# Optimization experiments

Hardware: AMD Instinct MI355X
Metric: run time of the kernel (lower is better)

The kernel has to match this reference:

```python
import jax, jax.numpy as jnp
import numpy as np

H = 8          # n_heads
C_FACTOR = 3   # autocorrelation factor c
KS = 25        # series-decomp moving-average kernel


def series_decomp(x, ks=KS):
    # AvgPool1d(kernel=ks, stride=1, pad=ks//2), count_include_pad=True (torch default)
    p = ks // 2
    xp = jnp.pad(x, ((0, 0), (p, p), (0, 0)))            # [B, L+2p, D]
    cs = jnp.pad(jnp.cumsum(xp, axis=1), ((0, 0), (1, 0), (0, 0)))
    trend = (cs[:, ks:, :] - cs[:, :-ks, :]) / ks         # [B, L, D]
    return x - trend, trend


def auto_correlation(x, Wq, bq, Wk, bk, Wv, bv):
    B, L, D = x.shape
    d = D // H

    def proj(W, b):  # [B,L,D] -> [B,H,L,d]
        return (x @ W + b).reshape(B, L, H, d).transpose(0, 2, 1, 3)

    Q, K, V = proj(Wq, bq), proj(Wk, bk), proj(Wv, bv)
    Qf = jnp.fft.rfft(Q, axis=2)
    Kf = jnp.fft.rfft(K, axis=2)
    Corr = jnp.fft.irfft(Qf * jnp.conj(Kf), n=L, axis=2)  # [B,H,L,d]

    k = int(C_FACTOR * np.log(L))                         # topk = int(c*log(L))
    C2 = Corr.transpose(0, 1, 3, 2)                       # [B,H,d,L] - topk along lag axis per channel
    W_topk, I_topk = jax.lax.top_k(C2, k)                 # [B,H,d,k]
    W_topk = jax.nn.softmax(W_topk, axis=-1)

    # saturating shift: pos = min(delay + t, L-1)  (faithful to clamp(max=L-1))
    t = jnp.arange(L)
    pos = jnp.minimum(I_topk[..., None] + t[None, None, None, None, :], L - 1)  # [B,H,d,k,L]
    Vt = V.transpose(0, 1, 3, 2)                          # [B,H,d,L]
    gathered = jnp.take_along_axis(Vt[:, :, :, None, :], pos, axis=4)           # [B,H,d,k,L]
    R = jnp.einsum('bhdk,bhdkl->bhdl', W_topk, gathered)  # weighted aggregate over lags
    return R.transpose(0, 3, 1, 2).reshape(B, L, D)       # [B,L,D]


def setup_inputs() -> dict:
    key = jax.random.key(0)
    ks = jax.random.split(key, 11)
    B, L, D = 8, 1024, 512
    s = 0.02
    return {
        'x':  jax.random.normal(ks[0], (B, L, D), jnp.float32),
        'Wq': jax.random.normal(ks[1], (D, D), jnp.float32) * s,
        'bq': jnp.zeros((D,), jnp.float32),
        'Wk': jax.random.normal(ks[2], (D, D), jnp.float32) * s,
        'bk': jnp.zeros((D,), jnp.float32),
        'Wv': jax.random.normal(ks[3], (D, D), jnp.float32) * s,
        'bv': jnp.zeros((D,), jnp.float32),
        'W1': jax.random.normal(ks[4], (D, D), jnp.float32) * s,
        'b1': jnp.zeros((D,), jnp.float32),
        'W2': jax.random.normal(ks[5], (D, D), jnp.float32) * s,
        'b2': jnp.zeros((D,), jnp.float32),
    }


def reference(x, Wq, bq, Wk, bk, Wv, bv, W1, b1, W2, b2):
    attn = auto_correlation(x, Wq, bq, Wk, bk, Wv, bv)
    x_s, _ = series_decomp(attn + x)
    y = jax.nn.relu(x_s @ W1 + b1) @ W2 + b2              # FFN (dropout is identity in eval)
    x_s, _ = series_decomp(y + x_s)
    return x_s
```

## Files before the change

### kernel.cpp

```cpp
#include <hip/hip_runtime.h>
#include <math.h>

#define LL 1024
#define DD 512
#define NB 8
#define KTOP 20
#define SZ (8 * 512 * 1024)

typedef __attribute__((ext_vector_type(8))) short bf16x8;
typedef __attribute__((ext_vector_type(4))) float f32x4;
typedef __attribute__((ext_vector_type(4))) int i32x4;

__device__ __forceinline__ unsigned short f2bf(float f) {
  union { float f; unsigned u; } v; v.f = f;
  unsigned r = v.u + 0x7FFFu + ((v.u >> 16) & 1u);
  return (unsigned short)(r >> 16);
}
__device__ __forceinline__ float bf2f(unsigned short u) {
  union { unsigned u; float f; } v; v.u = ((unsigned)u) << 16;
  return v.f;
}

__device__ __forceinline__ void gload16(const void* g, void* l) {
  __builtin_amdgcn_global_load_lds(
      (const __attribute__((address_space(1))) unsigned int*)g,
      (__attribute__((address_space(3))) unsigned int*)l, 16, 0, 0);
}

__global__ __launch_bounds__(256) void k_prep(const float* __restrict__ x,
                                              unsigned short* __restrict__ xbT,
                                              unsigned short* __restrict__ xb,
                                              const float* __restrict__ Wq,
                                              const float* __restrict__ Wk,
                                              const float* __restrict__ Wv,
                                              const float* __restrict__ W1,
                                              const float* __restrict__ W2,
                                              const float* __restrict__ bq,
                                              const float* __restrict__ bk,
                                              const float* __restrict__ bv,
                                              unsigned short* __restrict__ WqkvT,
                                              unsigned short* __restrict__ W1T,
                                              unsigned short* __restrict__ W2T,
                                              float* __restrict__ bqkv) {
  __shared__ float T[64][65];
  int bid = blockIdx.x;
  int tid = threadIdx.x;
  int lane = tid & 63, r4 = tid >> 6;
  if (bid < 1024) {
    int b = bid >> 7, c0 = ((bid >> 4) & 7) * 64, t0 = (bid & 15) * 64;
#pragma unroll
    for (int it = 0; it < 16; ++it) {
      int tl = it * 4 + r4;
      T[lane][tl] = x[((size_t)b * LL + t0 + tl) * DD + c0 + lane];
    }
    __syncthreads();
#pragma unroll
    for (int it = 0; it < 16; ++it) {
      int cl = it * 4 + r4;
      xbT[((size_t)b * DD + c0 + cl) * LL + t0 + lane] = f2bf(T[cl][lane]);
    }
    int tl2 = tid >> 2, cq = (tid & 3) * 16;
    unsigned short* dxb = xb + ((size_t)b * LL + t0 + tl2) * DD + c0 + cq;
#pragma unroll
    for (int j = 0; j < 16; j += 4) {
      ushort4 u;
      u.x = f2bf(T[cq + j][tl2]);
      u.y = f2bf(T[cq + j + 1][tl2]);
      u.z = f2bf(T[cq + j + 2][tl2]);
      u.w = f2bf(T[cq + j + 3][tl2]);
      *(ushort4*)&dxb[j] = u;
    }
  } else {
    int pid = bid - 1024;
    int z = pid >> 6, n0 = ((pid >> 3) & 7) * 64, k0 = (pid & 7) * 64;
    const float* W = (z == 0) ? Wq : (z == 1) ? Wk : (z == 2) ? Wv : (z == 3) ? W1 : W2;
    unsigned short* dst = (z == 0) ? WqkvT
                        : (z == 1) ? (WqkvT + 512 * 512)
                        : (z == 2) ? (WqkvT + 1024 * 512)
                        : (z == 3) ? W1T : W2T;
#pragma unroll
    for (int it = 0; it < 16; ++it) {
      int kl = it * 4 + r4;
      T[lane][kl] = W[(size_t)(k0 + kl) * DD + n0 + lane];
    }
    __syncthreads();
    int n = tid >> 2, kq = (tid & 3) * 16;
    unsigned short* d = dst + (size_t)(n0 + n) * DD + k0 + kq;
#pragma unroll
    for (int j = 0; j < 16; j += 4) {
      ushort4 u;
      u.x = f2bf(T[n][kq + j]);
      u.y = f2bf(T[n][kq + j + 1]);
      u.z = f2bf(T[n][kq + j + 2]);
      u.w = f2bf(T[n][kq + j + 3]);
      *(ushort4*)&d[j] = u;
    }
    if (z == 4 && n0 == 0 && k0 == 0) {
      for (int i = tid; i < 1536; i += 256) {
        const float* s = (i < 512) ? bq : (i < 1024) ? bk : bv;
        bqkv[i] = s[i & 511];
      }
    }
  }
}

template <int MODE, int BM>
__global__ __launch_bounds__(256) void k_mfma(const unsigned short* __restrict__ Aptr,
                                              const unsigned short* __restrict__ Bt,
                                              const float* __restrict__ bias,
                                              const unsigned short* __restrict__ resbT,
                                              unsigned short* __restrict__ outU,
                                              float* __restrict__ outF, int gx) {
  constexpr int MI = BM / 32;
  __shared__ char smem[(BM + 128) * 64 * 2 + (BM == 128 ? 2048 : 0)];
  unsigned short* As = (unsigned short*)smem;
  unsigned short* Bs = (unsigned short*)(smem + BM * 128);
  float* Cs = (float*)smem;

  int tid = threadIdx.x;
  int lane = tid & 63, wid = tid >> 6;
  int wr = wid & 1, wc = wid >> 1;

  int nwg = gridDim.x;
  int wg = blockIdx.x;
  int swz = (wg & 7) * (nwg >> 3) + (wg >> 3);
  int bix = swz % gx, biy = swz / gx;
  int n0 = bix * 128, m0 = biy * BM;
  int b = m0 >> 10, t0 = m0 & (LL - 1);

  f32x4 acc[MI][4];
#pragma unroll
  for (int i = 0; i < MI; ++i)
#pragma unroll
    for (int j = 0; j < 4; ++j) acc[i][j] = (f32x4){0.f, 0.f, 0.f, 0.f};

  int srow = tid >> 3, sq = tid & 7;

  for (int k0 = 0; k0 < 512; k0 += 64) {
#pragma unroll
    for (int p = 0; p < MI; ++p) {
      int r = srow + p * 32;
      int dq = sq ^ (r & 7);
      gload16(Aptr + (size_t)(m0 + r) * 512 + k0 + dq * 8, &As[r * 64 + sq * 8]);
    }
#pragma unroll
    for (int p = 0; p < 4; ++p) {
      int r = srow + p * 32;
      int dq = sq ^ (r & 7);
      gload16(Bt + (size_t)(n0 + r) * 512 + k0 + dq * 8, &Bs[r * 64 + sq * 8]);
    }
    __syncthreads();
#pragma unroll
    for (int ks = 0; ks < 2; ++ks) {
      bf16x8 af[MI], bf[4];
      int fr = lane & 15, kq = lane >> 4;
#pragma unroll
      for (int mi = 0; mi < MI; ++mi) {
        int r = wr * (BM / 2) + mi * 16 + fr;
        af[mi] = *(bf16x8*)&As[r * 64 + ((ks * 4 + kq) ^ (r & 7)) * 8];
      }
#pragma unroll
      for (int ni = 0; ni < 4; ++ni) {
        int r = wc * 64 + ni * 16 + fr;
        bf[ni] = *(bf16x8*)&Bs[r * 64 + ((ks * 4 + kq) ^ (r & 7)) * 8];
      }
#pragma unroll
      for (int mi = 0; mi < MI; ++mi)
#pragma unroll
        for (int ni = 0; ni < 4; ++ni)
          acc[mi][ni] = __builtin_amdgcn_mfma_f32_16x16x32_bf16(af[mi], bf[ni], acc[mi][ni], 0, 0, 0);
    }
    __syncthreads();
  }

  if (MODE == 0) {
    const int LDc = 132;
    for (int p = 0; p < 2; ++p) {
      __syncthreads();
      if (wc == p) {
#pragma unroll
        for (int mi = 0; mi < MI; ++mi)
#pragma unroll
          for (int ni = 0; ni < 4; ++ni) {
            int nl = ni * 16 + (lane & 15);
            int ml = wr * (BM / 2) + mi * 16 + (lane >> 4) * 4;
            *(f32x4*)&Cs[nl * LDc + ml] = acc[mi][ni];
          }
      }
      __syncthreads();
      {
        int n = tid >> 2, mq = tid & 3;
        int ng = n0 + p * 64 + n;
        float bv = bias[ng];
        int sel = ng >> 9;
        unsigned short* drow =
            outU + ((size_t)sel * NB * 512 + b * 512 + (ng & 511)) * LL + t0;
#pragma unroll
        for (int i = 0; i < 8; ++i) {
          int m = mq * 4 + i * 16;
          float4 v = *(float4*)&Cs[n * LDc + m];
          ushort4 u;
          u.x = f2bf(v.x + bv); u.y = f2bf(v.y + bv);
          u.z = f2bf(v.z + bv); u.w = f2bf(v.w + bv);
          *(ushort4*)&drow[m] = u;
        }
      }
    }
  } else if (MODE == 2) {
    const int LDc = 68;
    for (int p = 0; p < 2; ++p) {
      __syncthreads();
      {
        int n = tid >> 2, mq = tid & 3;
        const unsigned short* rrow =
            resbT + ((size_t)(b * 512) + n0 + p * 64 + n) * LL + t0;
#pragma unroll
        for (int i = 0; i < 4; ++i) {
          int m = mq * 16 + i * 4;
          ushort4 u = *(const ushort4*)&rrow[m];
          float4 v;
          v.x = bf2f(u.x); v.y = bf2f(u.y); v.z = bf2f(u.z); v.w = bf2f(u.w);
          *(float4*)&Cs[n * LDc + m] = v;
        }
      }
      __syncthreads();
      if (wc == p) {
#pragma unroll
        for (int mi = 0; mi < MI; ++mi)
#pragma unroll
          for (int ni = 0; ni < 4; ++ni) {
            int nl = ni * 16 + (lane & 15);
            int ml = wr * (BM / 2) + mi * 16 + (lane >> 4) * 4;
            f32x4 cur = *(f32x4*)&Cs[nl * LDc + ml];
            cur += acc[mi][ni];
            *(f32x4*)&Cs[nl * LDc + ml] = cur;
          }
      }
      __syncthreads();
      {
        int n = tid >> 2, mq = tid & 3;
        int ng = n0 + p * 64 + n;
        float bv = bias[ng];
        float* drow = outF + ((size_t)b * 512 + ng) * LL + t0;
#pragma unroll
        for (int i = 0; i < 4; ++i) {
          int m = mq * 16 + i * 4;
          float4 v = *(float4*)&Cs[n * LDc + m];
          v.x += bv; v.y += bv; v.z += bv; v.w += bv;
          *(float4*)&drow[m] = v;
        }
      }
    }
  } else {
    const int LDh = 68;
    for (int p = 0; p < 2; ++p) {
      __syncthreads();
      if (wc == p) {
#pragma unroll
        for (int mi = 0; mi < MI; ++mi)
#pragma unroll
          for (int ni = 0; ni < 4; ++ni) {
            int nl = ni * 16 + (lane & 15);
            int ml = wr * (BM / 2) + mi * 16 + (lane >> 4) * 4;
#pragma unroll
            for (int r = 0; r < 4; ++r) Cs[(ml + r) * LDh + nl] = acc[mi][ni][r];
          }
      }
      __syncthreads();
      {
        int m = tid >> 2, nh = tid & 3;
        unsigned short* drow =
            outU + (size_t)(m0 + m) * 512 + n0 + p * 64 + nh * 16;
#pragma unroll
        for (int c = 0; c < 4; ++c) {
          float4 v = *(float4*)&Cs[m * LDh + nh * 16 + c * 4];
          float4 bb = *(const float4*)&bias[n0 + p * 64 + nh * 16 + c * 4];
          v.x = fmaxf(v.x + bb.x, 0.f);
          v.y = fmaxf(v.y + bb.y, 0.f);
          v.z = fmaxf(v.z + bb.z, 0.f);
          v.w = fmaxf(v.w + bb.w, 0.f);
          ushort4 u;
          u.x = f2bf(v.x); u.y = f2bf(v.y); u.z = f2bf(v.z); u.w = f2bf(v.w);
          *(ushort4*)&drow[c * 4] = u;
        }
      }
    }
  }
}

__global__ __launch_bounds__(256, 8) void k_autocorr(const unsigned short* __restrict__ Qbf,
                                                     const unsigned short* __restrict__ Kbf,
                                                     const unsigned short* __restrict__ Vbf,
                                                     const unsigned short* __restrict__ xbT,
                                                     unsigned short* __restrict__ xsbT) {
  __shared__ char sm[16672];
  unsigned* KshW = (unsigned*)sm;
  float* Vs2 = (float*)(sm + 8320);
  float* wvs = (float*)(sm + 16512);
  int*   wis = (int*)(sm + 16592);
  float* Csp = (float*)sm;
  float* Cp  = (float*)(sm + 4224);

  int tid = threadIdx.x;
  int lane = tid & 63, wave = tid >> 6;
  size_t base = (size_t)blockIdx.x * LL;

  {
    ushort4 vv = *(const ushort4*)(Vbf + base + tid * 4);
    float4 vf;
    vf.x = bf2f(vv.x); vf.y = bf2f(vv.y); vf.z = bf2f(vv.z); vf.w = bf2f(vv.w);
    *(float4*)&Vs2[tid * 4] = vf;
    float vlast = bf2f(Vbf[base + 1023]);
    *(float4*)&Vs2[1024 + tid * 4] = make_float4(vlast, vlast, vlast, vlast);

    ushort4 kv = *(const ushort4*)(Kbf + base + tid * 4);
    unsigned w0 = (unsigned)kv.x | ((unsigned)kv.y << 16);
    unsigned w1 = (unsigned)kv.z | ((unsigned)kv.w << 16);
    unsigned wq = __shfl_up(w0, 1);
    unsigned wp = __shfl_up(w1, 1);
    if (lane == 0) {
      wq = *(const unsigned*)(Kbf + base + ((tid * 4 - 4) & (LL - 1)));
      wp = *(const unsigned*)(Kbf + base + ((tid * 4 - 2) & (LL - 1)));
    }
    int d = 8 + 2 * tid;
    uint2 u0; u0.x = w0;                      u0.y = w1;
    uint2 u1; u1.x = (wp >> 16) | (w0 << 16); u1.y = (w0 >> 16) | (w1 << 16);
    uint2 u2; u2.x = wp;                      u2.y = w0;
    uint2 u3; u3.x = (wq >> 16) | (wp << 16); u3.y = (wp >> 16) | (w0 << 16);
    *(uint2*)&KshW[d]        = u0;
    *(uint2*)&KshW[520 + d]  = u1;
    *(uint2*)&KshW[1040 + d] = u2;
    *(uint2*)&KshW[1560 + d] = u3;
    if (tid >= 224) {
      int q2 = tid - 224;
      int s = q2 >> 3, dd = q2 & 7;
      int p = 2 * dd - 16;
      unsigned short a = Kbf[base + ((p - s) & (LL - 1))];
      unsigned short b2 = Kbf[base + ((p + 1 - s) & (LL - 1))];
      KshW[s * 520 + dd] = (unsigned)a | ((unsigned)b2 << 16);
    }
  }
  __syncthreads();

  f32x4 acc = (f32x4){0.f, 0.f, 0.f, 0.f};
  int fr = lane & 15, kq = lane >> 4;
  int g = wave;
  int srow = fr & 3, fp = fr >> 2;
  int aE = (256 * g + 16 * fr + 8 * kq) & (LL - 1);
  int bD0 = srow * 520 + 8 + 4 * kq - 2 * fp;
  const unsigned short* qp = Qbf + base;
#pragma unroll
  for (int ks = 0; ks < 32; ++ks) {
    bf16x8 av = *(const bf16x8*)(qp + aE);
    int bD = bD0 + 16 * ks;
    uint2 b01 = *(const uint2*)&KshW[bD];
    uint2 b23 = *(const uint2*)&KshW[bD + 2];
    union { unsigned u[4]; bf16x8 h; } ub;
    ub.u[0] = b01.x; ub.u[1] = b01.y; ub.u[2] = b23.x; ub.u[3] = b23.y;
    acc = __builtin_amdgcn_mfma_f32_16x16x32_bf16(av, ub.h, acc, 0, 0, 0);
    aE = (aE + 32) & (LL - 1);
  }
  __syncthreads();
#pragma unroll
  for (int r = 0; r < 4; ++r) {
    int tau = 256 * g + 64 * kq + 16 * r + fr;
    Cp[tau ^ (((tau >> 6) & 3) << 4)] = acc[r];
  }
  __syncthreads();

  int sel = blockIdx.x & 3;
  if (wave == sel) {
    float c0[16];
#pragma unroll
    for (int j = 0; j < 16; ++j) {
      int tau = 64 * j + lane;
      c0[j] = Cp[tau ^ (((tau >> 6) & 3) << 4)];
    }
    float lbest = c0[0];
    int lidx = 0;
#pragma unroll
    for (int m = 1; m < 16; ++m)
      if (c0[m] > lbest) { lbest = c0[m]; lidx = m; }

#pragma unroll 1
    for (int s = 0; s < KTOP; ++s) {
      float best = lbest;
      int bidx = 64 * lidx + lane;
#pragma unroll
      for (int off = 32; off; off >>= 1) {
        float v2 = __shfl_xor(best, off);
        int i2 = __shfl_xor(bidx, off);
        if (v2 > best || (v2 == best && i2 < bidx)) { best = v2; bidx = i2; }
      }
      if (lane == 0) { wvs[s] = best; wis[s] = bidx; }
      int kill = ((bidx & 63) == lane) ? (bidx >> 6) : -1;
#pragma unroll
      for (int m = 0; m < 16; ++m)
        if (m == kill) c0[m] = -3.0e38f;
      lbest = c0[0];
      lidx = 0;
#pragma unroll
      for (int m = 1; m < 16; ++m)
        if (c0[m] > lbest) { lbest = c0[m]; lidx = m; }
    }
    float mx = wvs[0];
    float e = (lane < KTOP) ? __expf(wvs[lane] - mx) : 0.f;
    float ssum = e;
#pragma unroll
    for (int off = 32; off; off >>= 1) ssum += __shfl_xor(ssum, off);
    if (lane < KTOP) wvs[lane] = e / ssum;
  } else {
    int ft = (wave < sel ? wave : wave - 1) * 64 + lane;
    if (ft < 16) Csp[ft] = 0.f;
    else if (ft < 32) Csp[1040 + ft - 16] = 0.f;
  }
  __syncthreads();

  {
    float r[4];
#pragma unroll
    for (int i = 0; i < 4; ++i) r[i] = bf2f(xbT[base + tid + 256 * i]);
#pragma unroll
    for (int k = 0; k < KTOP; ++k) {
      float w = wvs[k];
      int wi = wis[k];
#pragma unroll
      for (int i = 0; i < 4; ++i) r[i] += w * Vs2[wi + tid + 256 * i];
    }
#pragma unroll
    for (int i = 0; i < 4; ++i) Csp[16 + tid + 256 * i] = r[i];
  }
  __syncthreads();

  {
    int t0 = tid * 4;
    float buf[28];
#pragma unroll
    for (int qd = 0; qd < 7; ++qd)
      *(float4*)&buf[qd * 4] = *(const float4*)&Csp[t0 + 4 + qd * 4];
    float s = 0.f;
#pragma unroll
    for (int m = 0; m < 25; ++m) s += buf[m];
    ushort4 o;
    o.x = f2bf(buf[12] - s * (1.0f / 25.0f));
    s += buf[25] - buf[0];
    o.y = f2bf(buf[13] - s * (1.0f / 25.0f));
    s += buf[26] - buf[1];
    o.z = f2bf(buf[14] - s * (1.0f / 25.0f));
    s += buf[27] - buf[2];
    o.w = f2bf(buf[15] - s * (1.0f / 25.0f));
    *(ushort4*)&xsbT[base + t0] = o;
  }
}

__global__ __launch_bounds__(256) void k_castT(const unsigned short* __restrict__ src,
                                               unsigned short* __restrict__ dst) {
  __shared__ unsigned short T[64][68];
  int b = blockIdx.z;
  int t0 = blockIdx.x * 64, c0 = blockIdx.y * 64;
  int tid = threadIdx.x;
  int lane = tid & 63, r4 = tid >> 6;
#pragma unroll
  for (int it = 0; it < 16; ++it) {
    int cl = it * 4 + r4;
    T[lane][cl] = src[((size_t)b * 512 + c0 + cl) * LL + t0 + lane];
  }
  __syncthreads();
  int tl = tid >> 2, cq = (tid & 3) * 16;
  unsigned short* d = dst + ((size_t)b * LL + t0 + tl) * 512 + c0 + cq;
#pragma unroll
  for (int j = 0; j < 16; j += 4) {
    ushort4 u;
    u.x = T[tl][cq + j]; u.y = T[tl][cq + j + 1];
    u.z = T[tl][cq + j + 2]; u.w = T[tl][cq + j + 3];
    *(ushort4*)&d[j] = u;
  }
}

#define DCH 32
__global__ __launch_bounds__(256) void k_decomp2T(const float* __restrict__ s2T,
                                                  float* __restrict__ out) {
  __shared__ float T[DCH][289];
  int b = blockIdx.z, c0 = blockIdx.y * DCH, t0 = blockIdx.x * 256;
  int tid = threadIdx.x;
  {
    int row = tid >> 3, j0 = tid & 7;
    const float* src = s2T + ((size_t)b * 512 + c0 + row) * LL;
#pragma unroll
    for (int i = 0; i < 9; ++i) {
      int col = (j0 + i * 8) * 4;
      int t = t0 - 16 + col;
      float4 v = make_float4(0.f, 0.f, 0.f, 0.f);
      if (t >= 0 && t < LL) v = *(const float4*)&src[t];
      *(float4*)&T[row][col] = v;
    }
  }
  __syncthreads();
  int c = tid & 31, tg = tid >> 5;
  float sum = 0.f;
  int basec = tg * 32 + 4;
#pragma unroll
  for (int j = 0; j < 25; ++j) sum += T[c][basec + j];
  float* orow = out + ((size_t)b * LL + t0 + tg * 32) * 512 + c0 + c;
#pragma unroll 1
  for (int s = 0; s < 32; ++s) {
    float center = T[c][tg * 32 + 16 + s];
    orow[(size_t)s * 512] = center - sum * (1.f / 25.f);
    sum += T[c][basec + 25 + s] - T[c][basec + s];
  }
}

extern "C" void kernel_launch(void* const* d_in, const int* in_sizes, int n_in,
                              void* d_out, int out_size, void* d_ws, size_t ws_size,
                              hipStream_t stream) {
  const float* x  = (const float*)d_in[0];
  const float* Wq = (const float*)d_in[1];
  const float* bq = (const float*)d_in[2];
  const float* Wk = (const float*)d_in[3];
  const float* bk = (const float*)d_in[4];
  const float* Wv = (const float*)d_in[5];
  const float* bv = (const float*)d_in[6];
  const float* W1 = (const float*)d_in[7];
  const float* b1 = (const float*)d_in[8];
  const float* W2 = (const float*)d_in[9];
  const float* b2 = (const float*)d_in[10];
  float* out = (float*)d_out;
  char* w = (char*)d_ws;

  unsigned short* xbT   = (unsigned short*)w;
  unsigned short* Qbf   = (unsigned short*)(w + (size_t)SZ * 4);
  unsigned short* Kbf   = Qbf + SZ;
  unsigned short* Vbf   = Kbf + SZ;
  unsigned short* WqkvT = (unsigned short*)(w + (size_t)SZ * 12);
  unsigned short* W1T   = WqkvT + 1536 * 512;
  unsigned short* W2T   = W1T + 512 * 512;
  float* bqkv           = (float*)(W2T + 512 * 512);
  unsigned short* xb    = (unsigned short*)(w + (size_t)SZ * 14);
  unsigned short* h1    = (unsigned short*)w;
  unsigned short* xsb   = (unsigned short*)(w + (size_t)SZ * 2);
  unsigned short* xsbT  = Qbf;
  float* s2T            = (float*)(w + (size_t)SZ * 6);

  k_prep<<<dim3(1344), 256, 0, stream>>>(x, xbT, xb, Wq, Wk, Wv, W1, W2,
                                         bq, bk, bv, WqkvT, W1T, W2T, bqkv);

  k_mfma<0, 128><<<dim3(768), 256, 0, stream>>>(xb, WqkvT, bqkv, nullptr, Qbf, nullptr, 12);

  k_autocorr<<<dim3(NB * DD), 256, 0, stream>>>(Qbf, Kbf, Vbf, xbT, xsbT);

  k_castT<<<dim3(16, 8, NB), 256, 0, stream>>>(xsbT, xsb);

  k_mfma<1, 64><<<dim3(512), 256, 0, stream>>>(xsb, W1T, b1, nullptr, h1, nullptr, 4);
  k_mfma<2, 64><<<dim3(512), 256, 0, stream>>>(h1, W2T, b2, xsbT, nullptr, s2T, 4);

  k_decomp2T<<<dim3(4, 16, NB), 256, 0, stream>>>(s2T, out);
}
```

Before: 136.6 us.

## Run per-wave top-k on MFMA registers and merge candidates in one wave

Instead of spilling the correlation tile to LDS and letting one wave scan all 1024 lags, each wave now runs its own top-20 over its 256 lags directly from the MFMA accumulators. The per-wave candidates are written to LDS and one wave merges the 80 candidates into the final top-20. The MFMA loop also splits accumulation across two accumulators to break the dependency chain. This removes a store/reload round trip and one barrier and parallelizes selection across four waves, at the cost of extra LDS and a second selection pass.

```diff
diff --git a/kernel.cpp b/kernel.cpp
--- a/kernel.cpp
+++ b/kernel.cpp
@@ -293,13 +293,14 @@
                                                      const unsigned short* __restrict__ Vbf,
                                                      const unsigned short* __restrict__ xbT,
                                                      unsigned short* __restrict__ xsbT) {
-  __shared__ char sm[16672];
+  __shared__ char sm[17312];
   unsigned* KshW = (unsigned*)sm;
   float* Vs2 = (float*)(sm + 8320);
-  float* wvs = (float*)(sm + 16512);
-  int*   wis = (int*)(sm + 16592);
+  float* cvs = (float*)(sm + 16512);
+  int*   cis = (int*)(sm + 16832);
+  float* wvs = (float*)(sm + 17152);
+  int*   wis = (int*)(sm + 17232);
   float* Csp = (float*)sm;
-  float* Cp  = (float*)(sm + 4224);
 
   int tid = threadIdx.x;
   int lane = tid & 63, wave = tid >> 6;
@@ -342,7 +343,8 @@
   }
   __syncthreads();
 
-  f32x4 acc = (f32x4){0.f, 0.f, 0.f, 0.f};
+  f32x4 acc0 = (f32x4){0.f, 0.f, 0.f, 0.f};
+  f32x4 acc1 = (f32x4){0.f, 0.f, 0.f, 0.f};
   int fr = lane & 15, kq = lane >> 4;
   int g = wave;
   int srow = fr & 3, fp = fr >> 2;
@@ -357,51 +359,72 @@
     uint2 b23 = *(const uint2*)&KshW[bD + 2];
     union { unsigned u[4]; bf16x8 h; } ub;
     ub.u[0] = b01.x; ub.u[1] = b01.y; ub.u[2] = b23.x; ub.u[3] = b23.y;
-    acc = __builtin_amdgcn_mfma_f32_16x16x32_bf16(av, ub.h, acc, 0, 0, 0);
+    if (ks & 1)
+      acc1 = __builtin_amdgcn_mfma_f32_16x16x32_bf16(av, ub.h, acc1, 0, 0, 0);
+    else
+      acc0 = __builtin_amdgcn_mfma_f32_16x16x32_bf16(av, ub.h, acc0, 0, 0, 0);
     aE = (aE + 32) & (LL - 1);
   }
-  __syncthreads();
-#pragma unroll
-  for (int r = 0; r < 4; ++r) {
-    int tau = 256 * g + 64 * kq + 16 * r + fr;
-    Cp[tau ^ (((tau >> 6) & 3) << 4)] = acc[r];
-  }
-  __syncthreads();
-
-  int sel = blockIdx.x & 3;
-  if (wave == sel) {
-    float c0[16];
-#pragma unroll
-    for (int j = 0; j < 16; ++j) {
-      int tau = 64 * j + lane;
-      c0[j] = Cp[tau ^ (((tau >> 6) & 3) << 4)];
-    }
-    float lbest = c0[0];
+
+  {
+    float c[4];
+    f32x4 at = acc0 + acc1;
+#pragma unroll
+    for (int r = 0; r < 4; ++r) c[r] = at[r];
+    int tb = 256 * g + 64 * kq + fr;
+
+    float lbest = c[0];
     int lidx = 0;
 #pragma unroll
-    for (int m = 1; m < 16; ++m)
-      if (c0[m] > lbest) { lbest = c0[m]; lidx = m; }
+    for (int m = 1; m < 4; ++m)
+      if (c[m] > lbest) { lbest = c[m]; lidx = m; }
 
 #pragma unroll 1
     for (int s = 0; s < KTOP; ++s) {
       float best = lbest;
-      int bidx = 64 * lidx + lane;
+      int btau = tb + 16 * lidx;
 #pragma unroll
       for (int off = 32; off; off >>= 1) {
         float v2 = __shfl_xor(best, off);
-        int i2 = __shfl_xor(bidx, off);
-        if (v2 > best || (v2 == best && i2 < bidx)) { best = v2; bidx = i2; }
-      }
-      if (lane == 0) { wvs[s] = best; wis[s] = bidx; }
-      int kill = ((bidx & 63) == lane) ? (bidx >> 6) : -1;
-#pragma unroll
-      for (int m = 0; m < 16; ++m)
-        if (m == kill) c0[m] = -3.0e38f;
-      lbest = c0[0];
+        int i2 = __shfl_xor(btau, off);
+        if (v2 > best || (v2 == best && i2 < btau)) { best = v2; btau = i2; }
+      }
+      if (lane == 0) { cvs[g * KTOP + s] = best; cis[g * KTOP + s] = btau; }
+      int owner = ((btau >> 6) & 3) * 16 + (btau & 15);
+      int kr = (lane == owner) ? ((btau >> 4) & 3) : -1;
+#pragma unroll
+      for (int m = 0; m < 4; ++m)
+        if (m == kr) c[m] = -3.0e38f;
+      lbest = c[0];
       lidx = 0;
 #pragma unroll
-      for (int m = 1; m < 16; ++m)
-        if (c0[m] > lbest) { lbest = c0[m]; lidx = m; }
+      for (int m = 1; m < 4; ++m)
+        if (c[m] > lbest) { lbest = c[m]; lidx = m; }
+    }
+  }
+  __syncthreads();
+
+  int sel = blockIdx.x & 3;
+  if (wave == sel) {
+    float m0v = cvs[lane];
+    int m0t = cis[lane];
+    float m1v = (lane < 16) ? cvs[64 + lane] : -3.0e38f;
+    int m1t = (lane < 16) ? cis[64 + lane] : 0x7fffffff;
+#pragma unroll 1
+    for (int s = 0; s < KTOP; ++s) {
+      float best;
+      int btau;
+      if (m0v > m1v || (m0v == m1v && m0t < m1t)) { best = m0v; btau = m0t; }
+      else { best = m1v; btau = m1t; }
+#pragma unroll
+      for (int off = 32; off; off >>= 1) {
+        float v2 = __shfl_xor(best, off);
+        int i2 = __shfl_xor(btau, off);
+        if (v2 > best || (v2 == best && i2 < btau)) { best = v2; btau = i2; }
+      }
+      if (lane == 0) { wvs[s] = best; wis[s] = btau; }
+      if (m0t == btau) m0v = -3.0e38f;
+      if (m1t == btau) m1v = -3.0e38f;
     }
     float mx = wvs[0];
     float e = (lane < KTOP) ? __expf(wvs[lane] - mx) : 0.f;
```

Measured after the change: 164.6 us. 1.21x slower.
